# Kernel optimization log

Hardware: AMD Instinct MI355X
Metric: run time of the kernel (lower is better)

Reference implementation:

```python
import jax, jax.numpy as jnp
import numpy as np

VOL_SHAPE = (192, 192, 192)
BATCH = 2
CHANNELS = 1


def setup_inputs() -> dict:
    key = jax.random.key(0)
    k1, k2 = jax.random.split(key)
    vol = jax.random.normal(k1, (BATCH,) + VOL_SHAPE + (CHANNELS,), dtype=jnp.float32)
    # near-identity affine (3,4) per batch element, as in rigid/affine motion correction
    eye = jnp.concatenate([jnp.eye(3, dtype=jnp.float32), jnp.zeros((3, 1), jnp.float32)], axis=1)
    affine = eye[None] + 0.02 * jax.random.normal(k2, (BATCH, 3, 4), dtype=jnp.float32)
    return {"vol": vol, "affine": affine}


def _warp(vol, affine):
    # vol: [B, D, H, W, C], affine: [B, 3, 4]
    B, D, H, W, C = vol.shape
    shape = (D, H, W)
    # --- affine_to_dense_shift (shift_center=True, ij indexing) ---
    ranges = [jnp.arange(s, dtype=jnp.float32) for s in shape]
    mesh = jnp.stack(jnp.meshgrid(*ranges, indexing='ij'), axis=-1)  # [D,H,W,3]
    center = jnp.array([(s - 1) / 2.0 for s in shape], dtype=jnp.float32)
    centered = mesh - center                                          # shifted grid
    homog = jnp.concatenate([centered, jnp.ones(shape + (1,), jnp.float32)], axis=-1)  # [D,H,W,4]
    loc_aff = jnp.einsum('bij,dhwj->bdhwi', affine, homog)            # [B,D,H,W,3]
    shift = loc_aff - centered                                        # dense warp field
    # --- SpatialTransformer: sample at grid + shift ---
    loc = mesh + shift                                                # [B,D,H,W,3]

    maxl = jnp.array([s - 1 for s in shape], dtype=jnp.float32)

    def interp_one(v, l):
        # v: [D,H,W,C], l: [D,H,W,3]; trilinear interp, clamp-to-edge (fill_value=None)
        cl = jnp.clip(l, 0.0, maxl)
        l0 = jnp.clip(jnp.floor(l), 0.0, maxl)
        l1 = jnp.clip(l0 + 1.0, 0.0, maxl)
        w_c0 = l1 - cl          # weight used with the floor corner (diff_loc1)
        w_c1 = 1.0 - w_c0       # weight used with the ceil corner  (diff_loc0)
        i0 = l0.astype(jnp.int32)
        i1 = l1.astype(jnp.int32)
        out = jnp.zeros(v.shape[:-1] + (v.shape[-1],), v.dtype)
        for c in range(8):  # 2^3 cube corners (fixed small loop)
            bits = ((c >> 2) & 1, (c >> 1) & 1, c & 1)
            idx = [(i1 if b else i0)[..., d] for d, b in enumerate(bits)]
            w = jnp.ones(l.shape[:-1], v.dtype)
            for d, b in enumerate(bits):
                w = w * (w_c1 if b else w_c0)[..., d]
            out = out + v[idx[0], idx[1], idx[2]] * w[..., None]
        return out

    return jax.vmap(interp_one)(vol, loc)


def reference(vol, affine):
    return _warp(vol, affine)
```

## Files before the change

### kernel.cpp

```cpp
#include <hip/hip_runtime.h>

#define DIM   192
#define PLANE (DIM * DIM)
#define NB    2
#define DPT   4
#define BH    4

typedef float f2 __attribute__((ext_vector_type(2), aligned(4)));

__global__ __launch_bounds__(256) __attribute__((amdgpu_waves_per_eu(4, 4))) void
SpatialTransformer_warp_kernel(const float* __restrict__ vol,
                               const float* __restrict__ affine,
                               float* __restrict__ out) {
    const int tid = threadIdx.x;
    const int w   = (blockIdx.x << 6) + (tid & 63);
    const int h   = blockIdx.y * BH + (tid >> 6);
    const int z   = blockIdx.z;
    const int b   = (z >= DIM / DPT) ? 1 : 0;
    const int d0  = (z - b * (DIM / DPT)) * DPT;

    const float* __restrict__ A = affine + b * 12;
    const float a00 = A[0], a01 = A[1], a02 = A[2],  a03 = A[3];
    const float a10 = A[4], a11 = A[5], a12 = A[6],  a13 = A[7];
    const float a20 = A[8], a21 = A[9], a22 = A[10], a23 = A[11];

    const float center = (DIM - 1) * 0.5f;
    const float maxl   = (float)(DIM - 1);
    const float maxi0  = (float)(DIM - 2);
    const float fplane = (float)PLANE;
    const float fdim   = (float)DIM;

    const float ch = (float)h - center;
    const float cw = (float)w - center;

    const float pd = a01 * ch + a02 * cw + a03 + center;
    const float ph = a11 * ch + a12 * cw + a13 + center;
    const float pw = a21 * ch + a22 * cw + a23 + center;

    const float* __restrict__ vb = vol + (size_t)b * DIM * PLANE;
    float* __restrict__ ob = out + ((size_t)b * DIM + d0) * PLANE
                                 + (size_t)h * DIM + w;

    f2 r00[DPT], r01[DPT], r10[DPT], r11[DPT];
    float w0d_[DPT], w0h_[DPT], w0w_[DPT];

#pragma unroll
    for (int k = 0; k < DPT; ++k) {
        const float cd = (float)(d0 + k) - center;
        const float ld = a00 * cd + pd;
        const float lh = a10 * cd + ph;
        const float lw = a20 * cd + pw;

        const float td = __builtin_amdgcn_fmed3f(ld, 0.0f, maxl);
        const float th = __builtin_amdgcn_fmed3f(lh, 0.0f, maxl);
        const float tw = __builtin_amdgcn_fmed3f(lw, 0.0f, maxl);

        const float fd = fminf(floorf(td), maxi0);
        const float fh = fminf(floorf(th), maxi0);
        const float fw = fminf(floorf(tw), maxi0);

        w0d_[k] = fd + 1.0f - td;
        w0h_[k] = fh + 1.0f - th;
        w0w_[k] = fw + 1.0f - tw;

        const int idx = (int)__builtin_fmaf(fd, fplane, __builtin_fmaf(fh, fdim, fw));
        const float* p = vb + idx;

        r00[k] = *(const f2*)(p);
        r01[k] = *(const f2*)(p + DIM);
        r10[k] = *(const f2*)(p + PLANE);
        r11[k] = *(const f2*)(p + PLANE + DIM);
    }

    __builtin_amdgcn_sched_barrier(0);

#pragma unroll
    for (int k = 0; k < DPT; ++k) {
        const float w0w = w0w_[k], w1w = 1.0f - w0w;
        const float w0h = w0h_[k], w1h = 1.0f - w0h;
        const float w0d = w0d_[k], w1d = 1.0f - w0d;

        const float x00 = r00[k].x * w0w + r00[k].y * w1w;
        const float x01 = r01[k].x * w0w + r01[k].y * w1w;
        const float x10 = r10[k].x * w0w + r10[k].y * w1w;
        const float x11 = r11[k].x * w0w + r11[k].y * w1w;

        const float y0 = x00 * w0h + x01 * w1h;
        const float y1 = x10 * w0h + x11 * w1h;

        __builtin_nontemporal_store(y0 * w0d + y1 * w1d, ob + k * PLANE);
    }
}

extern "C" void kernel_launch(void* const* d_in, const int* in_sizes, int n_in,
                              void* d_out, int out_size, void* d_ws, size_t ws_size,
                              hipStream_t stream) {
    const float* vol    = (const float*)d_in[0];
    const float* affine = (const float*)d_in[1];
    float* out = (float*)d_out;

    dim3 grid(DIM / 64, DIM / BH, NB * (DIM / DPT));
    dim3 block(256);
    SpatialTransformer_warp_kernel<<<grid, block, 0, stream>>>(vol, affine, out);
}
```

Baseline: 122.9 us.

## Assign four consecutive W outputs per thread and store them as one 16-byte vector

```diff
diff --git a/kernel.cpp b/kernel.cpp
--- a/kernel.cpp
+++ b/kernel.cpp
@@ -3,21 +3,25 @@
 #define DIM   192
 #define PLANE (DIM * DIM)
 #define NB    2
-#define DPT   4
-#define BH    4
+#define WPT   4
+#define BH    16
+#define BW    64
 
 typedef float f2 __attribute__((ext_vector_type(2), aligned(4)));
+typedef float f4v __attribute__((ext_vector_type(4), aligned(16)));
 
 __global__ __launch_bounds__(256) __attribute__((amdgpu_waves_per_eu(4, 4))) void
 SpatialTransformer_warp_kernel(const float* __restrict__ vol,
                                const float* __restrict__ affine,
                                float* __restrict__ out) {
     const int tid = threadIdx.x;
-    const int w   = (blockIdx.x << 6) + (tid & 63);
-    const int h   = blockIdx.y * BH + (tid >> 6);
+    const int l   = tid & 63;
+    const int wv  = tid >> 6;
+    const int w0  = blockIdx.x * BW + ((l & 15) << 2);
+    const int h   = blockIdx.y * BH + (wv << 2) + (l >> 4);
     const int z   = blockIdx.z;
-    const int b   = (z >= DIM / DPT) ? 1 : 0;
-    const int d0  = (z - b * (DIM / DPT)) * DPT;
+    const int b   = (z >= DIM) ? 1 : 0;
+    const int d   = z - b * DIM;
 
     const float* __restrict__ A = affine + b * 12;
     const float a00 = A[0], a01 = A[1], a02 = A[2],  a03 = A[3];
@@ -30,66 +34,66 @@
     const float fplane = (float)PLANE;
     const float fdim   = (float)DIM;
 
+    const float cd = (float)d - center;
     const float ch = (float)h - center;
-    const float cw = (float)w - center;
+    const float cw = (float)w0 - center;
 
-    const float pd = a01 * ch + a02 * cw + a03 + center;
-    const float ph = a11 * ch + a12 * cw + a13 + center;
-    const float pw = a21 * ch + a22 * cw + a23 + center;
+    const float pd = __builtin_fmaf(a00, cd, __builtin_fmaf(a01, ch, a03 + center));
+    const float ph = __builtin_fmaf(a10, cd, __builtin_fmaf(a11, ch, a13 + center));
+    const float pw = __builtin_fmaf(a20, cd, __builtin_fmaf(a21, ch, a23 + center));
 
     const float* __restrict__ vb = vol + (size_t)b * DIM * PLANE;
-    float* __restrict__ ob = out + ((size_t)b * DIM + d0) * PLANE
-                                 + (size_t)h * DIM + w;
+    float* __restrict__ ob = out + ((size_t)b * DIM + d) * PLANE
+                                 + (size_t)h * DIM + w0;
 
-    f2 r00[DPT], r01[DPT], r10[DPT], r11[DPT];
-    float w0d_[DPT], w0h_[DPT], w0w_[DPT];
+    f2 r00[WPT], r01[WPT], r10[WPT], r11[WPT];
+    float w0d_[WPT], w0h_[WPT], w0w_[WPT];
 
 #pragma unroll
-    for (int k = 0; k < DPT; ++k) {
-        const float cd = (float)(d0 + k) - center;
-        const float ld = a00 * cd + pd;
-        const float lh = a10 * cd + ph;
-        const float lw = a20 * cd + pw;
-
-        const float td = __builtin_amdgcn_fmed3f(ld, 0.0f, maxl);
-        const float th = __builtin_amdgcn_fmed3f(lh, 0.0f, maxl);
-        const float tw = __builtin_amdgcn_fmed3f(lw, 0.0f, maxl);
+    for (int i = 0; i < WPT; ++i) {
+        const float cwi = cw + (float)i;
+        const float td = __builtin_amdgcn_fmed3f(__builtin_fmaf(a02, cwi, pd), 0.0f, maxl);
+        const float th = __builtin_amdgcn_fmed3f(__builtin_fmaf(a12, cwi, ph), 0.0f, maxl);
+        const float tw = __builtin_amdgcn_fmed3f(__builtin_fmaf(a22, cwi, pw), 0.0f, maxl);
 
         const float fd = fminf(floorf(td), maxi0);
         const float fh = fminf(floorf(th), maxi0);
         const float fw = fminf(floorf(tw), maxi0);
 
-        w0d_[k] = fd + 1.0f - td;
-        w0h_[k] = fh + 1.0f - th;
-        w0w_[k] = fw + 1.0f - tw;
+        w0d_[i] = fd + 1.0f - td;
+        w0h_[i] = fh + 1.0f - th;
+        w0w_[i] = fw + 1.0f - tw;
 
         const int idx = (int)__builtin_fmaf(fd, fplane, __builtin_fmaf(fh, fdim, fw));
         const float* p = vb + idx;
 
-        r00[k] = *(const f2*)(p);
-        r01[k] = *(const f2*)(p + DIM);
-        r10[k] = *(const f2*)(p + PLANE);
-        r11[k] = *(const f2*)(p + PLANE + DIM);
+        r00[i] = *(const f2*)(p);
+        r01[i] = *(const f2*)(p + DIM);
+        r10[i] = *(const f2*)(p + PLANE);
+        r11[i] = *(const f2*)(p + PLANE + DIM);
     }
 
     __builtin_amdgcn_sched_barrier(0);
 
+    f4v res;
 #pragma unroll
-    for (int k = 0; k < DPT; ++k) {
-        const float w0w = w0w_[k], w1w = 1.0f - w0w;
-        const float w0h = w0h_[k], w1h = 1.0f - w0h;
-        const float w0d = w0d_[k], w1d = 1.0f - w0d;
+    for (int i = 0; i < WPT; ++i) {
+        const float w0w = w0w_[i], w1w = 1.0f - w0w;
+        const float w0h = w0h_[i], w1h = 1.0f - w0h;
+        const float w0d = w0d_[i], w1d = 1.0f - w0d;
 
-        const float x00 = r00[k].x * w0w + r00[k].y * w1w;
-        const float x01 = r01[k].x * w0w + r01[k].y * w1w;
-        const float x10 = r10[k].x * w0w + r10[k].y * w1w;
-        const float x11 = r11[k].x * w0w + r11[k].y * w1w;
+        const float x00 = r00[i].x * w0w + r00[i].y * w1w;
+        const float x01 = r01[i].x * w0w + r01[i].y * w1w;
+        const float x10 = r10[i].x * w0w + r10[i].y * w1w;
+        const float x11 = r11[i].x * w0w + r11[i].y * w1w;
 
         const float y0 = x00 * w0h + x01 * w1h;
         const float y1 = x10 * w0h + x11 * w1h;
 
-        __builtin_nontemporal_store(y0 * w0d + y1 * w1d, ob + k * PLANE);
+        res[i] = y0 * w0d + y1 * w1d;
     }
+
+    __builtin_nontemporal_store(res, (f4v*)ob);
 }
 
 extern "C" void kernel_launch(void* const* d_in, const int* in_sizes, int n_in,
@@ -99,7 +103,7 @@
     const float* affine = (const float*)d_in[1];
     float* out = (float*)d_out;
 
-    dim3 grid(DIM / 64, DIM / BH, NB * (DIM / DPT));
+    dim3 grid(DIM / BW, DIM / BH, NB * DIM);
     dim3 block(256);
     SpatialTransformer_warp_kernel<<<grid, block, 0, stream>>>(vol, affine, out);
 }
```

Result: no change. 124.7 us (+1.5%).
